# Kernel tuning notes

Hardware: AMD Instinct MI355X
Metric: run time of the kernel (lower is better)

The kernel has to match this reference:

```python
import jax, jax.numpy as jnp
import numpy as np

N_BLADES = 8  # Cl(3,0): 1, e1, e2, e3 and their products (bitmask blade indexing)


def _blade_sign(a: int, b: int) -> int:
    # Sign from reordering basis vectors when multiplying blades a*b (Euclidean metric).
    a >>= 1
    s = 0
    while a:
        s += bin(a & b).count('1')
        a >>= 1
    return -1 if (s & 1) else 1


def make_cayley() -> np.ndarray:
    C = np.zeros((N_BLADES, N_BLADES, N_BLADES), dtype=np.float32)
    for a in range(N_BLADES):
        for b in range(N_BLADES):
            C[a, b, a ^ b] = float(_blade_sign(a, b))
    return C


def setup_inputs() -> dict:
    key = jax.random.key(0)
    k1, k2 = jax.random.split(key)
    B, Cin, Cout = 8192, 256, 256
    scale = 1.0 / np.sqrt(Cin * N_BLADES)
    x = jax.random.normal(k1, (B, Cin, N_BLADES), dtype=jnp.float32)
    weight = jax.random.normal(k2, (Cout, Cin, N_BLADES), dtype=jnp.float32) * scale
    bias = jnp.zeros((Cout, N_BLADES), dtype=jnp.float32)
    cayley = jnp.asarray(make_cayley())
    return {"x": x, "weight": weight, "bias": bias, "cayley": cayley}


def reference(x, weight, bias, cayley):
    # A[b,o,j,k] = sum_i W[o,i,j] * X[b,i,k]  (weight blade j times input blade k)
    A = jnp.einsum('oij,bik->bojk', weight, x)
    # Contract blade pair (j,k) into output blade l via sparse Cayley table.
    out = jnp.einsum('jkl,bojk->bol', cayley, A)
    return out + bias[None, :, :]
```

## Files before the change

kernel.cpp:

```cpp
#include <hip/hip_runtime.h>
#include <stdint.h>
#include <stddef.h>


typedef __bf16 bf16x8  __attribute__((ext_vector_type(8)));
typedef float  f32x4   __attribute__((ext_vector_type(4)));

#define BM 128
#define BN 128
#define BK 32

__device__ __forceinline__ void async_copy16(void* lds_dst, const void* g_src) {
    __builtin_amdgcn_global_load_lds(
        (__attribute__((address_space(1))) void*)g_src,
        (__attribute__((address_space(3))) void*)lds_dst,
        16, 0, 0);
}

__global__ __launch_bounds__(256) void prep_kernel(
    const float* __restrict__ x, __bf16* __restrict__ Xb, long nx,
    const float* __restrict__ W, const float* __restrict__ cayley,
    __bf16* __restrict__ Wt, int Cin, int Cout, int castBlocks)
{
    __shared__ float Cay[512];
    if ((int)blockIdx.x < castBlocks) {
        long i = ((long)blockIdx.x * 256 + threadIdx.x) * 8;
        if (i + 8 <= nx) {
            const f32x4* p = (const f32x4*)(x + i);
            f32x4 v0 = p[0];
            f32x4 v1 = p[1];
            bf16x8 o;
            o[0] = (__bf16)v0[0]; o[1] = (__bf16)v0[1];
            o[2] = (__bf16)v0[2]; o[3] = (__bf16)v0[3];
            o[4] = (__bf16)v1[0]; o[5] = (__bf16)v1[1];
            o[6] = (__bf16)v1[2]; o[7] = (__bf16)v1[3];
            *(bf16x8*)(Xb + i) = o;
        }
        return;
    }
    for (int t = threadIdx.x; t < 512; t += 256) Cay[t] = cayley[t];
    __syncthreads();

    int flat = (blockIdx.x - castBlocks) * 256 + threadIdx.x;
    int total = Cout * 8 * Cin;
    if (flat >= total) return;
    int i = flat % Cin;
    int n = flat / Cin;
    int o = n >> 3, l = n & 7;

    const float* wrow = W + ((size_t)o * Cin + i) * 8;
    float w8[8];
    #pragma unroll
    for (int j = 0; j < 8; ++j) w8[j] = wrow[j];

    bf16x8 outv;
    #pragma unroll
    for (int k = 0; k < 8; ++k) {
        float s = 0.f;
        #pragma unroll
        for (int j = 0; j < 8; ++j) s += Cay[j * 64 + k * 8 + l] * w8[j];
        outv[k] = (__bf16)s;
    }
    *(bf16x8*)(Wt + (size_t)n * (Cin * 8) + i * 8) = outv;
}

__global__ __launch_bounds__(256, 4) void gemm_bt_kernel(
    const __bf16* __restrict__ A,
    const __bf16* __restrict__ Bt,
    const float*  __restrict__ bias,
    float* __restrict__ C,
    int M, int N, int K)
{
    __shared__ __align__(16) __bf16 As0[BM * BK];
    __shared__ __align__(16) __bf16 As1[BM * BK];
    __shared__ __align__(16) __bf16 Bs0[BN * BK];
    __shared__ __align__(16) __bf16 Bs1[BN * BK];

    const int tid  = threadIdx.x;
    const int wave = tid >> 6;
    const int lane = tid & 63;
    const int quad = lane >> 4;
    const int l16  = lane & 15;

    const int bid   = blockIdx.x;
    const int band  = (bid & 7) | ((bid >> 7) << 3);
    const int ncol  = (bid >> 3) & 15;
    const int mBase = band * BM;
    const int nBase = ncol * BN;

    const int srow = lane >> 2;
    const int sgrp = (lane & 3) ^ ((srow >> 1) & 3);

    const __bf16* gA0 = A  + (size_t)(mBase + (2 * wave + 0) * 16 + srow) * K + sgrp * 8;
    const __bf16* gA1 = A  + (size_t)(mBase + (2 * wave + 1) * 16 + srow) * K + sgrp * 8;
    const __bf16* gB0 = Bt + (size_t)(nBase + (2 * wave + 0) * 16 + srow) * K + sgrp * 8;
    const __bf16* gB1 = Bt + (size_t)(nBase + (2 * wave + 1) * 16 + srow) * K + sgrp * 8;
    const int cOff0 = (2 * wave + 0) * 512;
    const int cOff1 = (2 * wave + 1) * 512;

    const int wm = (wave >> 1) * 64;
    const int wn = (wave & 1) * 64;
    const int offq = (quad ^ ((l16 >> 1) & 3)) * 8;
    const int rowA = (wm + l16) * BK;
    const int rowB = (wn + l16) * BK;

    f32x4 acc[4][4] = {};

#define PREFETCH(BUFA, BUFB, KOFF)                       \
    do {                                                 \
        async_copy16(&BUFA[cOff0], gA0 + (KOFF));        \
        async_copy16(&BUFA[cOff1], gA1 + (KOFF));        \
        async_copy16(&BUFB[cOff0], gB0 + (KOFF));        \
        async_copy16(&BUFB[cOff1], gB1 + (KOFF));        \
    } while (0)

#define COMPUTE(BUFA, BUFB)                                               \
    do {                                                                  \
        const __bf16* fA = &BUFA[rowA] + offq;                            \
        const __bf16* fB = &BUFB[rowB] + offq;                            \
        bf16x8 af[4], bfr[4];                                             \
        _Pragma("unroll")                                                 \
        for (int mt = 0; mt < 4; ++mt)                                    \
            af[mt] = *(const bf16x8*)(fA + mt * 16 * BK);                 \
        _Pragma("unroll")                                                 \
        for (int nt = 0; nt < 4; ++nt)                                    \
            bfr[nt] = *(const bf16x8*)(fB + nt * 16 * BK);                \
        _Pragma("unroll")                                                 \
        for (int mt = 0; mt < 4; ++mt)                                    \
            _Pragma("unroll")                                             \
            for (int nt = 0; nt < 4; ++nt)                                \
                acc[mt][nt] = __builtin_amdgcn_mfma_f32_16x16x32_bf16(    \
                    af[mt], bfr[nt], acc[mt][nt], 0, 0, 0);               \
    } while (0)

    PREFETCH(As0, Bs0, 0);

    int k0 = 0;
    for (; k0 < K - 2 * BK; k0 += 2 * BK) {
        __syncthreads();
        PREFETCH(As1, Bs1, k0 + BK);
        COMPUTE(As0, Bs0);

        __syncthreads();
        PREFETCH(As0, Bs0, k0 + 2 * BK);
        COMPUTE(As1, Bs1);
    }

    __syncthreads();
    PREFETCH(As1, Bs1, k0 + BK);
    COMPUTE(As0, Bs0);

    __syncthreads();
    COMPUTE(As1, Bs1);

#undef PREFETCH
#undef COMPUTE

    float bv[4];
    #pragma unroll
    for (int nt = 0; nt < 4; ++nt)
        bv[nt] = bias[nBase + wn + nt * 16 + l16];

    #pragma unroll
    for (int mt = 0; mt < 4; ++mt) {
        #pragma unroll
        for (int nt = 0; nt < 4; ++nt) {
            const int col = nBase + wn + nt * 16 + l16;
            #pragma unroll
            for (int r = 0; r < 4; ++r) {
                const int row = mBase + wm + mt * 16 + quad * 4 + r;
                C[(size_t)row * N + col] = acc[mt][nt][r] + bv[nt];
            }
        }
    }
}

extern "C" void kernel_launch(void* const* d_in, const int* in_sizes, int n_in,
                              void* d_out, int out_size, void* d_ws, size_t ws_size,
                              hipStream_t stream) {
    const float* x      = (const float*)d_in[0];
    const float* weight = (const float*)d_in[1];
    const float* bias   = (const float*)d_in[2];
    const float* cayley = (const float*)d_in[3];
    float* out = (float*)d_out;

    const int Cout = in_sizes[2] / 8;
    const int Cin  = in_sizes[1] / (Cout * 8);
    const int Bm   = in_sizes[0] / (Cin * 8);
    const int M = Bm;
    const int N = Cout * 8;
    const int K = Cin * 8;

    __bf16* Xb = (__bf16*)d_ws;
    __bf16* Wt = (__bf16*)((char*)d_ws + (size_t)M * K * 2);

    long nx = (long)M * K;
    int castBlocks = (int)(nx / 8 / 256);
    int foldBlocks = (N * Cin + 255) / 256;
    prep_kernel<<<castBlocks + foldBlocks, 256, 0, stream>>>(
        x, Xb, nx, weight, cayley, Wt, Cin, Cout, castBlocks);

    int grid = (M / BM) * (N / BN);
    gemm_bt_kernel<<<grid, 256, 0, stream>>>(Xb, Wt, bias, out, M, N, K);
}
```

Measured before the change: 188.7 us.

## Pre-swizzle weights into MFMA fragment layout and load B directly from global

The weight-prep kernel now writes the folded weight matrix in a tiled layout that matches the MFMA B-fragment order, so each lane can read its 16-byte fragment straight from global memory. The GEMM drops the LDS buffers and async copies for B, keeping only A staged in LDS, and the block-to-tile mapping changes so consecutive blocks share a column tile. This removes LDS traffic and LDS footprint for B. In exchange, every wave issues its own B loads from global/L2 with no cross-wave reuse through LDS, and those loads sit directly on the compute critical path without prefetch.

```diff
diff --git a/kernel.cpp b/kernel.cpp
--- a/kernel.cpp
+++ b/kernel.cpp
@@ -61,40 +61,40 @@
         for (int j = 0; j < 8; ++j) s += Cay[j * 64 + k * 8 + l] * w8[j];
         outv[k] = (__bf16)s;
     }
-    *(bf16x8*)(Wt + (size_t)n * (Cin * 8) + i * 8) = outv;
+    const int K32 = Cin * 8 / 32;
+    size_t idx8 = (((size_t)(n >> 4) * K32 + (i >> 2)) * 4 + (i & 3)) * 16
+                  + (n & 15);
+    *(bf16x8*)(Wt + idx8 * 8) = outv;
 }
 
 __global__ __launch_bounds__(256, 4) void gemm_bt_kernel(
     const __bf16* __restrict__ A,
-    const __bf16* __restrict__ Bt,
+    const __bf16* __restrict__ Wt2,
     const float*  __restrict__ bias,
     float* __restrict__ C,
     int M, int N, int K)
 {
     __shared__ __align__(16) __bf16 As0[BM * BK];
     __shared__ __align__(16) __bf16 As1[BM * BK];
-    __shared__ __align__(16) __bf16 Bs0[BN * BK];
-    __shared__ __align__(16) __bf16 Bs1[BN * BK];
 
     const int tid  = threadIdx.x;
     const int wave = tid >> 6;
     const int lane = tid & 63;
     const int quad = lane >> 4;
     const int l16  = lane & 15;
+    const int K32  = K >> 5;
 
     const int bid   = blockIdx.x;
-    const int band  = (bid & 7) | ((bid >> 7) << 3);
-    const int ncol  = (bid >> 3) & 15;
+    const int band  = bid & 63;
+    const int ncol  = bid >> 6;
     const int mBase = band * BM;
     const int nBase = ncol * BN;
 
     const int srow = lane >> 2;
     const int sgrp = (lane & 3) ^ ((srow >> 1) & 3);
 
-    const __bf16* gA0 = A  + (size_t)(mBase + (2 * wave + 0) * 16 + srow) * K + sgrp * 8;
-    const __bf16* gA1 = A  + (size_t)(mBase + (2 * wave + 1) * 16 + srow) * K + sgrp * 8;
-    const __bf16* gB0 = Bt + (size_t)(nBase + (2 * wave + 0) * 16 + srow) * K + sgrp * 8;
-    const __bf16* gB1 = Bt + (size_t)(nBase + (2 * wave + 1) * 16 + srow) * K + sgrp * 8;
+    const __bf16* gA0 = A + (size_t)(mBase + (2 * wave + 0) * 16 + srow) * K + sgrp * 8;
+    const __bf16* gA1 = A + (size_t)(mBase + (2 * wave + 1) * 16 + srow) * K + sgrp * 8;
     const int cOff0 = (2 * wave + 0) * 512;
     const int cOff1 = (2 * wave + 1) * 512;
 
@@ -102,58 +102,62 @@
     const int wn = (wave & 1) * 64;
     const int offq = (quad ^ ((l16 >> 1) & 3)) * 8;
     const int rowA = (wm + l16) * BK;
-    const int rowB = (wn + l16) * BK;
+
+    const int tileN = (nBase + wn) >> 4;
+    const __bf16* pB[4];
+    #pragma unroll
+    for (int nt = 0; nt < 4; ++nt)
+        pB[nt] = Wt2 + ((((size_t)(tileN + nt) * K32) * 4 + quad) * 16 + l16) * 8;
 
     f32x4 acc[4][4] = {};
 
-#define PREFETCH(BUFA, BUFB, KOFF)                       \
+#define PREFETCH_A(BUFA, KOFF)                           \
     do {                                                 \
         async_copy16(&BUFA[cOff0], gA0 + (KOFF));        \
         async_copy16(&BUFA[cOff1], gA1 + (KOFF));        \
-        async_copy16(&BUFB[cOff0], gB0 + (KOFF));        \
-        async_copy16(&BUFB[cOff1], gB1 + (KOFF));        \
     } while (0)
 
-#define COMPUTE(BUFA, BUFB)                                               \
+#define COMPUTE(BUFA, KB)                                                 \
     do {                                                                  \
+        bf16x8 bfr[4];                                                    \
+        _Pragma("unroll")                                                 \
+        for (int nt = 0; nt < 4; ++nt)                                    \
+            bfr[nt] = *(const bf16x8*)(pB[nt] + (size_t)(KB) * 512);      \
         const __bf16* fA = &BUFA[rowA] + offq;                            \
-        const __bf16* fB = &BUFB[rowB] + offq;                            \
-        bf16x8 af[4], bfr[4];                                             \
+        bf16x8 af[4];                                                     \
         _Pragma("unroll")                                                 \
         for (int mt = 0; mt < 4; ++mt)                                    \
             af[mt] = *(const bf16x8*)(fA + mt * 16 * BK);                 \
         _Pragma("unroll")                                                 \
         for (int nt = 0; nt < 4; ++nt)                                    \
-            bfr[nt] = *(const bf16x8*)(fB + nt * 16 * BK);                \
-        _Pragma("unroll")                                                 \
-        for (int mt = 0; mt < 4; ++mt)                                    \
             _Pragma("unroll")                                             \
-            for (int nt = 0; nt < 4; ++nt)                                \
+            for (int mt = 0; mt < 4; ++mt)                                \
                 acc[mt][nt] = __builtin_amdgcn_mfma_f32_16x16x32_bf16(    \
                     af[mt], bfr[nt], acc[mt][nt], 0, 0, 0);               \
     } while (0)
 
-    PREFETCH(As0, Bs0, 0);
+    PREFETCH_A(As0, 0);
 
     int k0 = 0;
-    for (; k0 < K - 2 * BK; k0 += 2 * BK) {
+    int kb = 0;
+    for (; k0 < K - 2 * BK; k0 += 2 * BK, kb += 2) {
         __syncthreads();
-        PREFETCH(As1, Bs1, k0 + BK);
-        COMPUTE(As0, Bs0);
+        PREFETCH_A(As1, k0 + BK);
+        COMPUTE(As0, kb);
 
         __syncthreads();
-        PREFETCH(As0, Bs0, k0 + 2 * BK);
-        COMPUTE(As1, Bs1);
+        PREFETCH_A(As0, k0 + 2 * BK);
+        COMPUTE(As1, kb + 1);
     }
 
     __syncthreads();
-    PREFETCH(As1, Bs1, k0 + BK);
-    COMPUTE(As0, Bs0);
+    PREFETCH_A(As1, k0 + BK);
+    COMPUTE(As0, kb);
 
     __syncthreads();
-    COMPUTE(As1, Bs1);
-
-#undef PREFETCH
+    COMPUTE(As1, kb + 1);
+
+#undef PREFETCH_A
 #undef COMPUTE
 
     float bv[4];
```

Result: slower. 204.5 us (+8.4%).
